# Optimization experiments

Measured on AMD Instinct MI355X. Metric: run time of the kernel, lower is better.

The kernel has to match this reference:

```python
import jax, jax.numpy as jnp
import numpy as np

HEADS = 16
LN_EPS = 1e-5


def setup_inputs() -> dict:
    key = jax.random.key(0)
    ks = jax.random.split(key, 12)
    B, IMG, Q, H = 8192, 2048, 768, 1024
    def init(k, shape, fan_in):
        return jax.random.normal(k, shape, dtype=jnp.float32) * (fan_in ** -0.5)
    return {
        "features1": jax.random.normal(ks[0], (B, IMG), dtype=jnp.float32),
        "features2": jax.random.normal(ks[1], (B, Q), dtype=jnp.float32),
        "W1": init(ks[2], (IMG, H), IMG),
        "b1": jnp.zeros((H,), dtype=jnp.float32),
        "W2": init(ks[3], (Q, H), Q),
        "b2": jnp.zeros((H,), dtype=jnp.float32),
        "Wqkv": init(ks[4], (H, 3 * H), H),
        "Wout": init(ks[5], (H, H), H),
        "bout": jnp.zeros((H,), dtype=jnp.float32),
        "gamma": jnp.ones((2 * H,), dtype=jnp.float32),
        "beta": jnp.zeros((2 * H,), dtype=jnp.float32),
    }


def reference(features1, features2, W1, b1, W2, b2, Wqkv, Wout, bout, gamma, beta):
    B = features1.shape[0]
    H = W1.shape[1]
    hd = H // HEADS
    scale = hd ** -0.5
    # modality projections -> [B, H] each
    f1 = features1 @ W1 + b1
    f2 = features2 @ W2 + b2
    x = jnp.stack([f1, f2], axis=1)                      # [B, 2, H]
    qkv = x @ Wqkv                                       # [B, 2, 3H]
    q, k, v = jnp.split(qkv, 3, axis=-1)
    # b n (h d) -> b h n d
    def to_heads(t):
        return t.reshape(B, 2, HEADS, hd).transpose(0, 2, 1, 3)
    q, k, v = to_heads(q) * scale, to_heads(k), to_heads(v)
    attn = jnp.einsum('bhid,bhjd->bhij', q, k)           # [B, h, 2, 2]
    attn = jax.nn.softmax(attn, axis=-1)
    out = jnp.einsum('bhij,bhjd->bhid', attn, v)         # [B, h, 2, d]
    out = out.transpose(0, 2, 1, 3).reshape(B, 2, H)     # b h n d -> b n (h d)
    out = out @ Wout + bout                              # [B, 2, H]
    flat = out.reshape(B, 2 * H)
    # LayerNorm over last dim
    mu = jnp.mean(flat, axis=-1, keepdims=True)
    var = jnp.var(flat, axis=-1, keepdims=True)
    normed = (flat - mu) * jax.lax.rsqrt(var + LN_EPS) * gamma + beta
    # dropout in eval mode = identity
    res = jnp.concatenate([f1, f2], axis=1)              # [B, 2H]
    return normed + res
```

## Files before the change

kernel.cpp:

```cpp
#include <hip/hip_runtime.h>
#include <hip/hip_bf16.h>
#include <cstdint>

typedef __attribute__((ext_vector_type(8))) short short8;
typedef __attribute__((ext_vector_type(4))) short short4v;
typedef __attribute__((ext_vector_type(4))) float floatx4;
typedef __attribute__((ext_vector_type(4))) unsigned short ushort4v;

__device__ __forceinline__ float bf2f(unsigned short u) {
    union { unsigned int u; float f; } v;
    v.u = ((unsigned int)u) << 16;
    return v.f;
}
__device__ __forceinline__ unsigned short f2bf(float f) {
    union { float f; unsigned int u; } v; v.f = f;
    unsigned int u = v.u;
    unsigned int r = (u + 0x7FFFu + ((u >> 16) & 1u)) >> 16;
    return (unsigned short)r;
}
__device__ __forceinline__ float lo_bf(unsigned int u) {
    union { unsigned int u; float f; } v; v.u = u << 16; return v.f;
}
__device__ __forceinline__ float hi_bf(unsigned int u) {
    union { unsigned int u; float f; } v; v.u = u & 0xffff0000u; return v.f;
}
__device__ __forceinline__ void gld_lds16(const void* g, void* l) {
    __builtin_amdgcn_global_load_lds(
        (const __attribute__((address_space(1))) unsigned int*)g,
        (__attribute__((address_space(3))) unsigned int*)l,
        16, 0, 0);
}

__global__ __launch_bounds__(256) void prep_kernel(
    const float* __restrict__ f1, const float* __restrict__ f2,
    unsigned short* __restrict__ f1b, unsigned short* __restrict__ f2b,
    const float* __restrict__ W1, unsigned short* __restrict__ W1t,
    const float* __restrict__ W2, unsigned short* __restrict__ W2t,
    const float* __restrict__ Wqkv, unsigned short* __restrict__ Wqkvt,
    const float* __restrict__ Wout, unsigned short* __restrict__ Woutt) {
    __shared__ float tile[64][33];
    const int b = blockIdx.x;
    const int tid = threadIdx.x;

    if (b < 5632) {
        const float* in = (b < 4096) ? f1 : f2;
        unsigned short* outp = (b < 4096) ? f1b : f2b;
        int base = ((b < 4096) ? b : (b - 4096)) * 1024 + tid;
#pragma unroll
        for (int it = 0; it < 4; it++) {
            int i = base + it * 256;
            float4 v = ((const float4*)in)[i];
            ushort4v o;
            o.x = f2bf(v.x); o.y = f2bf(v.y); o.z = f2bf(v.z); o.w = f2bf(v.w);
            ((ushort4v*)outp)[i] = o;
        }
        return;
    }

    const float* in; unsigned short* outp; int K, N, t;
    if (b < 6656)      { in = W1;   outp = W1t;   K = 2048; N = 1024; t = b - 5632; }
    else if (b < 7040) { in = W2;   outp = W2t;   K = 768;  N = 1024; t = b - 6656; }
    else if (b < 8576) { in = Wqkv; outp = Wqkvt; K = 1024; N = 3072; t = b - 7040; }
    else               { in = Wout; outp = Woutt; K = 1024; N = 1024; t = b - 8576; }
    const int ntiles = N >> 5;
    const int n0 = (t % ntiles) * 32;
    const int k0 = (t / ntiles) * 64;
    const int tx = tid & 31, tg = tid >> 5;
#pragma unroll
    for (int i = 0; i < 8; i++)
        tile[tg * 8 + i][tx] = in[(size_t)(k0 + tg * 8 + i) * N + n0 + tx];
    __syncthreads();
    const int n = tid >> 3, kc = (tid & 7) * 8;
    short8 o;
#pragma unroll
    for (int j = 0; j < 8; j++) o[j] = (short)f2bf(tile[kc + j][n]);
    *(short8*)&outp[(size_t)(n0 + n) * K + k0 + kc] = o;
}

template <bool OUT_BF16, bool HAS_BIAS>
__device__ __forceinline__ void gemm_core(const unsigned short* __restrict__ A,
                                          const unsigned short* __restrict__ Bt,
                                          void* __restrict__ Cv, const float* __restrict__ bias,
                                          int K, int ldc, int blockM, int blockN,
                                          unsigned short* As, unsigned short* Bs) {
    const int tid  = threadIdx.x;
    const int lane = tid & 63;
    const int wave = tid >> 6;
    const int wm = wave >> 1, wn = wave & 1;

    const int kx = (tid >> 3) & 3;
    const unsigned short* gA = A  + (size_t)(blockM + (tid >> 2)) * K + ((tid & 3) ^ kx) * 8;
    const unsigned short* gB = Bt + (size_t)(blockN + (tid >> 2)) * K + ((tid & 3) ^ kx) * 8;
    const size_t sK = (size_t)64 * K;
    unsigned short* lA = As + wave * 512;
    unsigned short* lB = Bs + wave * 512;

    floatx4 acc[4][4];
#pragma unroll
    for (int i = 0; i < 4; i++)
#pragma unroll
        for (int j = 0; j < 4; j++) acc[i][j] = (floatx4){0.f, 0.f, 0.f, 0.f};

    const int col  = lane & 15;
    const int quad = lane >> 4;
    const int qx = quad ^ ((col >> 1) & 3);
    const int aoff32 = (wm * 64 + col) * 32 + qx * 8;
    const int boff32 = (wn * 64 + col) * 32 + qx * 8;

    const int kIters = K >> 6;
    for (int kt = 0; kt < kIters; ++kt) {
        const size_t ko = (size_t)kt * 64;
        gld_lds16(gA + ko,           lA);
        gld_lds16(gA + sK + ko,      lA + 2048);
        gld_lds16(gA + 32 + ko,      lA + 4096);
        gld_lds16(gA + sK + 32 + ko, lA + 6144);
        gld_lds16(gB + ko,           lB);
        gld_lds16(gB + sK + ko,      lB + 2048);
        gld_lds16(gB + 32 + ko,      lB + 4096);
        gld_lds16(gB + sK + 32 + ko, lB + 6144);
        __syncthreads();

#pragma unroll
        for (int hh = 0; hh < 2; hh++) {
            short8 a[4];
#pragma unroll
            for (int i = 0; i < 4; i++) a[i] = *(const short8*)&As[hh * 4096 + aoff32 + i * 512];
#pragma unroll
            for (int j = 0; j < 4; j++) {
                short8 bj = *(const short8*)&Bs[hh * 4096 + boff32 + j * 512];
#pragma unroll
                for (int i = 0; i < 4; i++)
                    acc[i][j] = __builtin_amdgcn_mfma_f32_16x16x32_bf16(a[i], bj, acc[i][j], 0, 0, 0);
            }
        }
        __syncthreads();
    }

#pragma unroll
    for (int i = 0; i < 4; i++) {
#pragma unroll
        for (int j = 0; j < 4; j++) {
#pragma unroll
            for (int r = 0; r < 4; r++) {
                int row = blockM + wm * 64 + i * 16 + quad * 4 + r;
                int cn  = blockN + wn * 64 + j * 16 + col;
                float v = acc[i][j][r];
                if (HAS_BIAS) v += bias[cn];
                if (OUT_BF16) ((unsigned short*)Cv)[(size_t)row * ldc + cn] = f2bf(v);
                else          ((float*)Cv)[(size_t)row * ldc + cn] = v;
            }
        }
    }
}

__global__ __launch_bounds__(256, 4)
void gemm_f12(const unsigned short* __restrict__ f1b, const unsigned short* __restrict__ W1t,
              const float* __restrict__ b1,
              const unsigned short* __restrict__ f2b, const unsigned short* __restrict__ W2t,
              const float* __restrict__ b2, unsigned short* __restrict__ xb) {
    __shared__ alignas(16) unsigned short As[8192];
    __shared__ alignas(16) unsigned short Bs[8192];
    const int blockM = blockIdx.x * 128;
    const int blockN = blockIdx.y * 128;
    if (blockIdx.z == 0)
        gemm_core<true, true>(f1b, W1t, (void*)xb, b1, 2048, 2048, blockM, blockN, As, Bs);
    else
        gemm_core<true, true>(f2b, W2t, (void*)(xb + 1024), b2, 768, 2048, blockM, blockN, As, Bs);
}

__global__ __launch_bounds__(256, 4)
void gemm_proj(const unsigned short* __restrict__ attn, const unsigned short* __restrict__ Woutt,
               const float* __restrict__ bout, unsigned short* __restrict__ projb) {
    __shared__ alignas(16) unsigned short As[8192];
    __shared__ alignas(16) unsigned short Bs[8192];
    gemm_core<true, true>(attn, Woutt, (void*)projb, bout, 1024, 1024,
                          blockIdx.x * 128, blockIdx.y * 128, As, Bs);
}

#define T2_STRIDE 132
__global__ __launch_bounds__(256, 3)
void gemm_qkv_attn(const unsigned short* __restrict__ A, const unsigned short* __restrict__ Bt,
                   unsigned short* __restrict__ attn_out) {
    __shared__ alignas(16) char smem[52224];
    unsigned short* As = (unsigned short*)smem;
    unsigned short* Bs = As + 8192;
    unsigned short* T2 = (unsigned short*)smem;
    float* wsm = (float*)(smem + 50688);

    const int tid  = threadIdx.x;
    const int lane = tid & 63;
    const int wave = tid >> 6;
    const int g = blockIdx.x;
    const int h = g >> 7;
    const int blockM = (g & 127) * 128;
    const int wm = wave >> 1, wn = wave & 1;
    const int K = 1024;

    const int kx = (tid >> 3) & 3;
    const unsigned short* gA = A  + (size_t)(blockM + (tid >> 2)) * K + ((tid & 3) ^ kx) * 8;
    const unsigned short* gB = Bt + (size_t)(h * 64 + (tid >> 2)) * K + ((tid & 3) ^ kx) * 8;
    unsigned short* lA = As + wave * 512;
    unsigned short* lB = Bs + wave * 512;

    floatx4 acc[4][6];
#pragma unroll
    for (int i = 0; i < 4; i++)
#pragma unroll
        for (int j = 0; j < 6; j++) acc[i][j] = (floatx4){0.f, 0.f, 0.f, 0.f};

    const int col  = lane & 15;
    const int quad = lane >> 4;
    const int qx = quad ^ ((col >> 1) & 3);
    const int aoff32 = (wm * 64 + col) * 32 + qx * 8;
    const int boff32 = (wn * 96 + col) * 32 + qx * 8;

    for (int kt = 0; kt < 16; ++kt) {
        const size_t ko = (size_t)kt * 64;
        gld_lds16(gA + ko,               lA);
        gld_lds16(gA + 65536 + ko,       lA + 2048);
        gld_lds16(gA + 32 + ko,          lA + 4096);
        gld_lds16(gA + 65536 + 32 + ko,  lA + 6144);
        gld_lds16(gB + ko,               lB);
        gld_lds16(gB + 1048576 + ko,     lB + 2048);
        gld_lds16(gB + 2097152 + ko,     lB + 4096);
        gld_lds16(gB + 32 + ko,          lB + 6144);
        gld_lds16(gB + 1048576 + 32 + ko, lB + 8192);
        gld_lds16(gB + 2097152 + 32 + ko, lB + 10240);
        __syncthreads();

#pragma unroll
        for (int hh = 0; hh < 2; hh++) {
            short8 a[4];
#pragma unroll
            for (int i = 0; i < 4; i++) a[i] = *(const short8*)&As[hh * 4096 + aoff32 + i * 512];
#pragma unroll
            for (int j = 0; j < 6; j++) {
                short8 bj = *(const short8*)&Bs[hh * 6144 + boff32 + j * 512];
#pragma unroll
                for (int i = 0; i < 4; i++)
                    acc[i][j] = __builtin_amdgcn_mfma_f32_16x16x32_bf16(a[i], bj, acc[i][j], 0, 0, 0);
            }
        }
        __syncthreads();
    }

#pragma unroll
    for (int i = 0; i < 4; i++) {
#pragma unroll
        for (int j = 0; j < 6; j++) {
            int c  = wn * 96 + j * 16 + col;
            int r0 = wm * 64 + i * 16 + quad * 4;
            short4v pk;
            pk.x = (short)f2bf(acc[i][j][0]);
            pk.y = (short)f2bf(acc[i][j][1]);
            pk.z = (short)f2bf(acc[i][j][2]);
            pk.w = (short)f2bf(acc[i][j][3]);
            *(short4v*)&T2[c * T2_STRIDE + r0] = pk;
        }
    }
    __syncthreads();

    if (tid < 64) {
        const int ib = tid;
        float s00 = 0.f, s01 = 0.f, s10 = 0.f, s11 = 0.f;
#pragma unroll 8
        for (int d = 0; d < 64; d++) {
            unsigned int qp = *(const unsigned int*)&T2[d * T2_STRIDE + 2 * ib];
            unsigned int kp = *(const unsigned int*)&T2[(64 + d) * T2_STRIDE + 2 * ib];
            float q0 = lo_bf(qp), q1 = hi_bf(qp);
            float k0 = lo_bf(kp), k1 = hi_bf(kp);
            s00 += q0 * k0; s01 += q0 * k1;
            s10 += q1 * k0; s11 += q1 * k1;
        }
        const float sc = 0.125f;
        s00 *= sc; s01 *= sc; s10 *= sc; s11 *= sc;
        float m0 = fmaxf(s00, s01), m1 = fmaxf(s10, s11);
        float e00 = __expf(s00 - m0), e01 = __expf(s01 - m0);
        float e10 = __expf(s10 - m1), e11 = __expf(s11 - m1);
        float i0 = 1.f / (e00 + e01), i1 = 1.f / (e10 + e11);
        wsm[ib * 4 + 0] = e00 * i0; wsm[ib * 4 + 1] = e01 * i0;
        wsm[ib * 4 + 2] = e10 * i1; wsm[ib * 4 + 3] = e11 * i1;
    }
    __syncthreads();

#pragma unroll
    for (int gg = 0; gg < 4; gg++) {
        int chunk = gg * 256 + tid;
        int r = chunk >> 3;
        int dc = (chunk & 7) * 8;
        int ib = r >> 1, n = r & 1;
        float w0 = wsm[ib * 4 + n * 2 + 0];
        float w1 = wsm[ib * 4 + n * 2 + 1];
        short8 o;
#pragma unroll
        for (int dd = 0; dd < 8; dd++) {
            unsigned int vp = *(const unsigned int*)&T2[(128 + dc + dd) * T2_STRIDE + 2 * ib];
            o[dd] = (short)f2bf(w0 * lo_bf(vp) + w1 * hi_bf(vp));
        }
        *(short8*)&attn_out[(size_t)(blockM + r) * 1024 + h * 64 + dc] = o;
    }
}

__global__ __launch_bounds__(256) void ln_res_kernel(const unsigned short* __restrict__ proj,
                                                     const unsigned short* __restrict__ xres,
                                                     const float* __restrict__ gamma,
                                                     const float* __restrict__ beta,
                                                     float* __restrict__ out) {
    const int b = blockIdx.x;
    const int tid = threadIdx.x;
    const size_t base = (size_t)b * 2048;
    short8 p8 = ((const short8*)(proj + base))[tid];
    float pv[8];
#pragma unroll
    for (int e = 0; e < 8; e++) pv[e] = bf2f((unsigned short)p8[e]);
    float s = 0.f, ss = 0.f;
#pragma unroll
    for (int e = 0; e < 8; e++) { s += pv[e]; ss += pv[e] * pv[e]; }
#pragma unroll
    for (int off = 32; off > 0; off >>= 1) {
        s  += __shfl_xor(s, off);
        ss += __shfl_xor(ss, off);
    }
    __shared__ float red[8];
    const int wave = tid >> 6;
    if ((tid & 63) == 0) { red[wave] = s; red[4 + wave] = ss; }
    __syncthreads();
    s  = red[0] + red[1] + red[2] + red[3];
    ss = red[4] + red[5] + red[6] + red[7];
    const float mean = s * (1.0f / 2048.0f);
    const float var  = ss * (1.0f / 2048.0f) - mean * mean;
    const float rstd = rsqrtf(var + 1e-5f);

    const float4* g4 = (const float4*)gamma;
    const float4* b4 = (const float4*)beta;
    float4 g0 = g4[2 * tid], g1 = g4[2 * tid + 1];
    float4 be0 = b4[2 * tid], be1 = b4[2 * tid + 1];
    short8 r8 = ((const short8*)(xres + base))[tid];
    float4 o0, o1;
    o0.x = (pv[0] - mean) * rstd * g0.x + be0.x + bf2f((unsigned short)r8[0]);
    o0.y = (pv[1] - mean) * rstd * g0.y + be0.y + bf2f((unsigned short)r8[1]);
    o0.z = (pv[2] - mean) * rstd * g0.z + be0.z + bf2f((unsigned short)r8[2]);
    o0.w = (pv[3] - mean) * rstd * g0.w + be0.w + bf2f((unsigned short)r8[3]);
    o1.x = (pv[4] - mean) * rstd * g1.x + be1.x + bf2f((unsigned short)r8[4]);
    o1.y = (pv[5] - mean) * rstd * g1.y + be1.y + bf2f((unsigned short)r8[5]);
    o1.z = (pv[6] - mean) * rstd * g1.z + be1.z + bf2f((unsigned short)r8[6]);
    o1.w = (pv[7] - mean) * rstd * g1.w + be1.w + bf2f((unsigned short)r8[7]);
    float4* op = (float4*)(out + base);
    op[2 * tid] = o0;
    op[2 * tid + 1] = o1;
}

extern "C" void kernel_launch(void* const* d_in, const int* in_sizes, int n_in,
                              void* d_out, int out_size, void* d_ws, size_t ws_size,
                              hipStream_t stream) {
    (void)in_sizes; (void)n_in; (void)out_size; (void)ws_size;
    const float* features1 = (const float*)d_in[0];
    const float* features2 = (const float*)d_in[1];
    const float* W1   = (const float*)d_in[2];
    const float* b1   = (const float*)d_in[3];
    const float* W2   = (const float*)d_in[4];
    const float* b2   = (const float*)d_in[5];
    const float* Wqkv = (const float*)d_in[6];
    const float* Wout = (const float*)d_in[7];
    const float* bout = (const float*)d_in[8];
    const float* gamma = (const float*)d_in[9];
    const float* beta  = (const float*)d_in[10];
    float* out = (float*)d_out;

    char* ws = (char*)d_ws;
    unsigned short* f1b   = (unsigned short*)(ws);
    unsigned short* f2b   = (unsigned short*)(ws + 33554432);
    unsigned short* W1t   = (unsigned short*)(ws + 46137344);
    unsigned short* W2t   = (unsigned short*)(ws + 50331648);
    unsigned short* Wqkvt = (unsigned short*)(ws + 51904512);
    unsigned short* Woutt = (unsigned short*)(ws + 58195968);
    unsigned short* xb    = (unsigned short*)(ws + 60293120);
    unsigned short* attn  = (unsigned short*)(ws + 93847552);
    unsigned short* projb = (unsigned short*)(ws + 127401984);

    prep_kernel<<<9088, 256, 0, stream>>>(features1, features2, f1b, f2b,
                                          W1, W1t, W2, W2t, Wqkv, Wqkvt, Wout, Woutt);
    gemm_f12<<<dim3(64, 8, 2), 256, 0, stream>>>(f1b, W1t, b1, f2b, W2t, b2, xb);
    gemm_qkv_attn<<<2048, 256, 0, stream>>>(xb, Wqkvt, attn);
    gemm_proj<<<dim3(128, 8), 256, 0, stream>>>(attn, Woutt, bout, projb);
    ln_res_kernel<<<8192, 256, 0, stream>>>(projb, xb, gamma, beta, out);
}
```

Before: 369.8 us.

## Fuse fp32-to-bf16 activation conversion into first projection GEMM

Removes the separate pass that converted features1/features2 from fp32 to bf16 in a workspace buffer. The first projection GEMM now loads fp32 A tiles into registers, converts them with packed bf16 conversion instructions, and writes them to LDS itself. The next tile's loads are issued during the MFMA loop to hide latency. This saves a full read-write round trip over the activations, at the cost of more registers (occupancy hint lowered from 4 to 3) and double the A-side global bandwidth inside the GEMM.

```diff
diff --git a/kernel.cpp b/kernel.cpp
--- a/kernel.cpp
+++ b/kernel.cpp
@@ -6,6 +6,7 @@
 typedef __attribute__((ext_vector_type(4))) short short4v;
 typedef __attribute__((ext_vector_type(4))) float floatx4;
 typedef __attribute__((ext_vector_type(4))) unsigned short ushort4v;
+typedef __attribute__((ext_vector_type(4))) unsigned int uint4v;
 
 __device__ __forceinline__ float bf2f(unsigned short u) {
     union { unsigned int u; float f; } v;
@@ -30,10 +31,13 @@
         (__attribute__((address_space(3))) unsigned int*)l,
         16, 0, 0);
 }
+__device__ __forceinline__ unsigned int cvtpk_bf16(float lo, float hi) {
+    unsigned int r;
+    asm("v_cvt_pk_bf16_f32 %0, %1, %2" : "=v"(r) : "v"(lo), "v"(hi));
+    return r;
+}
 
 __global__ __launch_bounds__(256) void prep_kernel(
-    const float* __restrict__ f1, const float* __restrict__ f2,
-    unsigned short* __restrict__ f1b, unsigned short* __restrict__ f2b,
     const float* __restrict__ W1, unsigned short* __restrict__ W1t,
     const float* __restrict__ W2, unsigned short* __restrict__ W2t,
     const float* __restrict__ Wqkv, unsigned short* __restrict__ Wqkvt,
@@ -42,26 +46,11 @@
     const int b = blockIdx.x;
     const int tid = threadIdx.x;
 
-    if (b < 5632) {
-        const float* in = (b < 4096) ? f1 : f2;
-        unsigned short* outp = (b < 4096) ? f1b : f2b;
-        int base = ((b < 4096) ? b : (b - 4096)) * 1024 + tid;
-#pragma unroll
-        for (int it = 0; it < 4; it++) {
-            int i = base + it * 256;
-            float4 v = ((const float4*)in)[i];
-            ushort4v o;
-            o.x = f2bf(v.x); o.y = f2bf(v.y); o.z = f2bf(v.z); o.w = f2bf(v.w);
-            ((ushort4v*)outp)[i] = o;
-        }
-        return;
-    }
-
     const float* in; unsigned short* outp; int K, N, t;
-    if (b < 6656)      { in = W1;   outp = W1t;   K = 2048; N = 1024; t = b - 5632; }
-    else if (b < 7040) { in = W2;   outp = W2t;   K = 768;  N = 1024; t = b - 6656; }
-    else if (b < 8576) { in = Wqkv; outp = Wqkvt; K = 1024; N = 3072; t = b - 7040; }
-    else               { in = Wout; outp = Woutt; K = 1024; N = 1024; t = b - 8576; }
+    if (b < 1024)      { in = W1;   outp = W1t;   K = 2048; N = 1024; t = b; }
+    else if (b < 1408) { in = W2;   outp = W2t;   K = 768;  N = 1024; t = b - 1024; }
+    else if (b < 2944) { in = Wqkv; outp = Wqkvt; K = 1024; N = 3072; t = b - 1408; }
+    else               { in = Wout; outp = Woutt; K = 1024; N = 1024; t = b - 2944; }
     const int ntiles = N >> 5;
     const int n0 = (t % ntiles) * 32;
     const int k0 = (t / ntiles) * 64;
@@ -153,19 +142,102 @@
     }
 }
 
-__global__ __launch_bounds__(256, 4)
-void gemm_f12(const unsigned short* __restrict__ f1b, const unsigned short* __restrict__ W1t,
+__global__ __launch_bounds__(256, 3)
+void gemm_f12(const float* __restrict__ f1, const unsigned short* __restrict__ W1t,
               const float* __restrict__ b1,
-              const unsigned short* __restrict__ f2b, const unsigned short* __restrict__ W2t,
+              const float* __restrict__ f2, const unsigned short* __restrict__ W2t,
               const float* __restrict__ b2, unsigned short* __restrict__ xb) {
     __shared__ alignas(16) unsigned short As[8192];
     __shared__ alignas(16) unsigned short Bs[8192];
+    const int tid  = threadIdx.x;
+    const int lane = tid & 63;
+    const int wave = tid >> 6;
+    const int wm = wave >> 1, wn = wave & 1;
     const int blockM = blockIdx.x * 128;
     const int blockN = blockIdx.y * 128;
-    if (blockIdx.z == 0)
-        gemm_core<true, true>(f1b, W1t, (void*)xb, b1, 2048, 2048, blockM, blockN, As, Bs);
-    else
-        gemm_core<true, true>(f2b, W2t, (void*)(xb + 1024), b2, 768, 2048, blockM, blockN, As, Bs);
+
+    const float* A; const unsigned short* Bt; const float* bias; int K; unsigned short* Cp;
+    if (blockIdx.z == 0) { A = f1; Bt = W1t; bias = b1; K = 2048; Cp = xb; }
+    else                 { A = f2; Bt = W2t; bias = b2; K = 768;  Cp = xb + 1024; }
+
+    const int kx = (tid >> 3) & 3;
+    const int srow = tid >> 2;
+    const int sc8  = ((tid & 3) ^ kx) * 8;
+    const float* gA = A + (size_t)(blockM + srow) * K + sc8;
+    const unsigned short* gB = Bt + (size_t)(blockN + srow) * K + sc8;
+    const size_t sK = (size_t)64 * K;
+    unsigned short* lB = Bs + wave * 512;
+    const int awbase = wave * 512 + lane * 8;
+
+    floatx4 acc[4][4];
+#pragma unroll
+    for (int i = 0; i < 4; i++)
+#pragma unroll
+        for (int j = 0; j < 4; j++) acc[i][j] = (floatx4){0.f, 0.f, 0.f, 0.f};
+
+    const int col  = lane & 15;
+    const int quad = lane >> 4;
+    const int qx = quad ^ ((col >> 1) & 3);
+    const int aoff32 = (wm * 64 + col) * 32 + qx * 8;
+    const int boff32 = (wn * 64 + col) * 32 + qx * 8;
+
+    float4 af[4][2];
+#define ISSUE_A(ko) do { \
+    af[0][0] = *(const float4*)(gA + (ko));           af[0][1] = *(const float4*)(gA + (ko) + 4); \
+    af[1][0] = *(const float4*)(gA + sK + (ko));      af[1][1] = *(const float4*)(gA + sK + (ko) + 4); \
+    af[2][0] = *(const float4*)(gA + 32 + (ko));      af[2][1] = *(const float4*)(gA + 32 + (ko) + 4); \
+    af[3][0] = *(const float4*)(gA + sK + 32 + (ko)); af[3][1] = *(const float4*)(gA + sK + 32 + (ko) + 4); } while (0)
+
+    const int kIters = K >> 6;
+    ISSUE_A(0);
+    for (int kt = 0; kt < kIters; ++kt) {
+        const size_t ko = (size_t)kt * 64;
+        gld_lds16(gB + ko,           lB);
+        gld_lds16(gB + sK + ko,      lB + 2048);
+        gld_lds16(gB + 32 + ko,      lB + 4096);
+        gld_lds16(gB + sK + 32 + ko, lB + 6144);
+#pragma unroll
+        for (int s = 0; s < 4; s++) {
+            uint4v pk;
+            pk.x = cvtpk_bf16(af[s][0].x, af[s][0].y);
+            pk.y = cvtpk_bf16(af[s][0].z, af[s][0].w);
+            pk.z = cvtpk_bf16(af[s][1].x, af[s][1].y);
+            pk.w = cvtpk_bf16(af[s][1].z, af[s][1].w);
+            *(uint4v*)&As[s * 2048 + awbase] = pk;
+        }
+        __syncthreads();
+
+#pragma unroll
+        for (int hh = 0; hh < 2; hh++) {
+            short8 a[4];
+#pragma unroll
+            for (int i = 0; i < 4; i++) a[i] = *(const short8*)&As[hh * 4096 + aoff32 + i * 512];
+#pragma unroll
+            for (int j = 0; j < 4; j++) {
+                short8 bj = *(const short8*)&Bs[hh * 4096 + boff32 + j * 512];
+#pragma unroll
+                for (int i = 0; i < 4; i++)
+                    acc[i][j] = __builtin_amdgcn_mfma_f32_16x16x32_bf16(a[i], bj, acc[i][j], 0, 0, 0);
+            }
+        }
+        if (kt + 1 < kIters) ISSUE_A(ko + 64);
+        __syncthreads();
+    }
+#undef ISSUE_A
+
+#pragma unroll
+    for (int i = 0; i < 4; i++) {
+#pragma unroll
+        for (int j = 0; j < 4; j++) {
+#pragma unroll
+            for (int r = 0; r < 4; r++) {
+                int row = blockM + wm * 64 + i * 16 + quad * 4 + r;
+                int cn  = blockN + wn * 64 + j * 16 + col;
+                float v = acc[i][j][r] + bias[cn];
+                Cp[(size_t)row * 2048 + cn] = f2bf(v);
+            }
+        }
+    }
 }
 
 __global__ __launch_bounds__(256, 4)
@@ -368,8 +440,6 @@
     float* out = (float*)d_out;
 
     char* ws = (char*)d_ws;
-    unsigned short* f1b   = (unsigned short*)(ws);
-    unsigned short* f2b   = (unsigned short*)(ws + 33554432);
     unsigned short* W1t   = (unsigned short*)(ws + 46137344);
     unsigned short* W2t   = (unsigned short*)(ws + 50331648);
     unsigned short* Wqkvt = (unsigned short*)(ws + 51904512);
@@ -378,9 +448,8 @@
     unsigned short* attn  = (unsigned short*)(ws + 93847552);
     unsigned short* projb = (unsigned short*)(ws + 127401984);
 
-    prep_kernel<<<9088, 256, 0, stream>>>(features1, features2, f1b, f2b,
-                                          W1, W1t, W2, W2t, Wqkv, Wqkvt, Wout, Woutt);
-    gemm_f12<<<dim3(64, 8, 2), 256, 0, stream>>>(f1b, W1t, b1, f2b, W2t, b2, xb);
+    prep_kernel<<<3456, 256, 0, stream>>>(W1, W1t, W2, W2t, Wqkv, Wqkvt, Wout, Woutt);
+    gemm_f12<<<dim3(64, 8, 2), 256, 0, stream>>>(features1, W1t, b1, features2, W2t, b2, xb);
     gemm_qkv_attn<<<2048, 256, 0, stream>>>(xb, Wqkvt, attn);
     gemm_proj<<<dim3(128, 8), 256, 0, stream>>>(attn, Woutt, bout, projb);
     ln_res_kernel<<<8192, 256, 0, stream>>>(projb, xb, gamma, beta, out);
```

Result: no change. 373.3 us (+0.9%).
